# Performance work log

Hardware: AMD Instinct MI355X
Metric: run time of the kernel (lower is better)

## Reference

```python
import jax, jax.numpy as jnp
import numpy as np

TEMPERATURE = 0.07
NEG_INF = -1e9


def setup_inputs() -> dict:
    key = jax.random.key(0)
    k1, k2, k3, k4, k5 = jax.random.split(key, 5)
    B, L, H = 64, 256, 64
    query_embs = jax.random.normal(k1, (B, L, H), dtype=jnp.float32)
    key_embs = jax.random.normal(k2, (B, L, H), dtype=jnp.float32)
    labels = jax.random.randint(k3, (B,), 0, 2, dtype=jnp.int64)
    q_mask = jax.random.randint(k4, (B, L), 0, 2, dtype=jnp.int32)
    k_mask = jax.random.randint(k5, (B, L), 0, 2, dtype=jnp.int32)
    return {"query_embs": query_embs, "key_embs": key_embs, "labels": labels,
            "q_mask": q_mask, "k_mask": k_mask}


def reference(query_embs, key_embs, labels, q_mask, k_mask):
    # ColBERT-style late interaction over all B x B pairs.
    # sim: (B_q, B_k, Lq, Lk) token-level dot products.
    sim = jnp.einsum('bqh,ckh->bcqk', query_embs, key_embs)
    # Mask out padded key tokens before the max over key positions.
    sim = jnp.where(k_mask[None, :, None, :].astype(bool), sim, NEG_INF)
    maxsim = jnp.max(sim, axis=-1)                      # (B_q, B_k, Lq)
    qm = q_mask[:, None, :].astype(maxsim.dtype)        # (B_q, 1, Lq)
    scores = jnp.sum(maxsim * qm, axis=-1) / TEMPERATURE  # (B_q, B_k)
    # Cross-entropy on rows with labels==1, target = diagonal index.
    logp = jax.nn.log_softmax(scores, axis=-1)
    B = scores.shape[0]
    diag = logp[jnp.arange(B), jnp.arange(B)]           # (B,)
    w = labels.astype(scores.dtype)
    denom = jnp.maximum(jnp.sum(w), 1.0)
    return -jnp.sum(w * diag) / denom
```

## Files before the change

kernel.cpp:

```cpp
#include <hip/hip_runtime.h>
#include <math.h>

#define PB 64
#define PL 256
#define PH 64
#define TEMP 0.07f
#define NEG_INF_F (-1e9f)

#define KSTRIDE 72
#define KROWB   (KSTRIDE * 2)
#define KSLAB   (PL * KSTRIDE)
#define BGRP    4

typedef short short8 __attribute__((ext_vector_type(8)));
typedef float f32x4 __attribute__((ext_vector_type(4)));

__device__ __forceinline__ unsigned short f32_to_bf16(float f) {
    unsigned int u = __float_as_uint(f);
    u += 0x7FFFu + ((u >> 16) & 1u);
    return (unsigned short)(u >> 16);
}

__global__ __launch_bounds__(256)
void prep_kernel(const float* __restrict__ Q,
                 const float* __restrict__ K,
                 const int*   __restrict__ kmask,
                 unsigned short* __restrict__ Qb,
                 unsigned short* __restrict__ Kcomp,
                 int* __restrict__ nvK) {
    const int tid = threadIdx.x;

    if (blockIdx.x >= 256) {
        const int bb      = blockIdx.x - 256;
        const int b       = bb >> 2;
        const int quarter = bb & 3;
        const float4* src = (const float4*)(Q + (size_t)b * PL * PH) + quarter * 1024;
        unsigned short* dst = Qb + (size_t)b * PL * PH + quarter * 4096;
        #pragma unroll
        for (int it = 0; it < 4; ++it) {
            int i = it * 256 + tid;
            float4 v = src[i];
            ushort4 o;
            o.x = f32_to_bf16(v.x); o.y = f32_to_bf16(v.y);
            o.z = f32_to_bf16(v.z); o.w = f32_to_bf16(v.w);
            *(ushort4*)(dst + (size_t)i * 4) = o;
        }
        return;
    }

    const int c       = blockIdx.x >> 2;
    const int quarter = blockIdx.x & 3;
    const int lane = tid & 63;
    const int wave = tid >> 6;
    __shared__ int posArr[PL];
    __shared__ int wcnt[4];

    const int km = kmask[c * PL + tid];
    unsigned long long bal = __ballot(km != 0);
    int within = __popcll(bal & ((1ull << lane) - 1ull));
    if (lane == 0) wcnt[wave] = __popcll(bal);
    __syncthreads();
    int base = 0;
    #pragma unroll
    for (int w = 0; w < 4; ++w) base += (w < wave) ? wcnt[w] : 0;
    posArr[tid] = km ? (base + within) : -1;
    const int nv = wcnt[0] + wcnt[1] + wcnt[2] + wcnt[3];
    __syncthreads();

    unsigned short* slab = Kcomp + (size_t)c * KSLAB;
    const int sub = lane >> 4;
    const int cl  = lane & 15;

    #pragma unroll
    for (int it = 0; it < 4; ++it) {
        int r = quarter * 64 + it * 16 + wave * 4 + sub;
        int p = posArr[r];
        if (p >= 0) {
            float4 v = *(const float4*)(K + ((size_t)c * PL + r) * PH + cl * 4);
            ushort4 o;
            o.x = f32_to_bf16(v.x); o.y = f32_to_bf16(v.y);
            o.z = f32_to_bf16(v.z); o.w = f32_to_bf16(v.w);
            *(ushort4*)(slab + (size_t)p * KSTRIDE + cl * 4) = o;
        }
    }

    const int rows16 = (nv + 15) & ~15;
    const int padChunks = (rows16 - nv) * 16;
    if (tid < padChunks) {
        int row = nv + (tid >> 4);
        if (row >= quarter * 64 && row < quarter * 64 + 64) {
            *(ushort4*)(slab + (size_t)row * KSTRIDE + (tid & 15) * 4) = (ushort4){0, 0, 0, 0};
        }
    }
    if (quarter == 0 && tid == 0) nvK[c] = nv;
}

__global__ __launch_bounds__(256)
void colbert_scores_mfma(const unsigned short* __restrict__ Qb,
                         const unsigned short* __restrict__ Kcomp,
                         const int*   __restrict__ nvK,
                         const int*   __restrict__ qmask,
                         float*       __restrict__ scores) {
    const int c  = blockIdx.x;
    const int bg = blockIdx.y;
    const int tid  = threadIdx.x;
    const int wave = tid >> 6;
    const int lane = tid & 63;
    const int n    = lane & 15;
    const int g    = (lane >> 4) & 3;

    __shared__ __align__(16) unsigned short Ks[PL * KSTRIDE];
    __shared__ float red[BGRP][4];

    const int nv     = nvK[c];
    const int rows16 = (nv + 15) & ~15;
    const int nbytes = rows16 * KROWB;

    {
        const char* gsrc  = (const char*)(Kcomp + (size_t)c * KSLAB);
        char*       lbase = (char*)Ks;
        const int nchunks = (nbytes + 4095) >> 12;
        for (int it = 0; it < nchunks; ++it) {
            int off = it * 4096 + tid * 16;
            __builtin_amdgcn_global_load_lds(
                (const __attribute__((address_space(1))) unsigned int*)(gsrc + off),
                (__attribute__((address_space(3)))       unsigned int*)(lbase + off),
                16, 0, 0);
        }
    }

    __syncthreads();

    const f32x4 ZERO4 = (f32x4){0.f, 0.f, 0.f, 0.f};
    const int ntFull   = nv >> 4;
    const int tailCols = nv & 15;
    const int qw0 = wave * 64;
    const unsigned short* krow0 = &Ks[n * KSTRIDE + g * 8];

    #pragma unroll 1
    for (int bi = 0; bi < BGRP; ++bi) {
        const int b = bg * BGRP + bi;

        short8 afrag[4][2];
        {
            const unsigned short* Qrow = Qb + ((size_t)b * PL) * PH;
            #pragma unroll
            for (int rt = 0; rt < 4; ++rt) {
                const unsigned short* p = Qrow + (size_t)(qw0 + rt * 16 + n) * PH + g * 8;
                afrag[rt][0] = *(const short8*)(p);
                afrag[rt][1] = *(const short8*)(p + 32);
            }
        }

        float maxv[4][4];
        #pragma unroll
        for (int rt = 0; rt < 4; ++rt)
            #pragma unroll
            for (int r = 0; r < 4; ++r) maxv[rt][r] = NEG_INF_F;

        int ct = 0;
        for (; ct + 1 < ntFull; ct += 2) {
            const unsigned short* ka = krow0 + ct * 16 * KSTRIDE;
            short8 kA0 = *(const short8*)(ka);
            short8 kA1 = *(const short8*)(ka + 32);
            short8 kB0 = *(const short8*)(ka + 16 * KSTRIDE);
            short8 kB1 = *(const short8*)(ka + 16 * KSTRIDE + 32);

            f32x4 accA[4], accB[4];
            #pragma unroll
            for (int rt = 0; rt < 4; ++rt) {
                accA[rt] = __builtin_amdgcn_mfma_f32_16x16x32_bf16(afrag[rt][0], kA0, ZERO4, 0, 0, 0);
                accB[rt] = __builtin_amdgcn_mfma_f32_16x16x32_bf16(afrag[rt][0], kB0, ZERO4, 0, 0, 0);
            }
            #pragma unroll
            for (int rt = 0; rt < 4; ++rt) {
                accA[rt] = __builtin_amdgcn_mfma_f32_16x16x32_bf16(afrag[rt][1], kA1, accA[rt], 0, 0, 0);
                accB[rt] = __builtin_amdgcn_mfma_f32_16x16x32_bf16(afrag[rt][1], kB1, accB[rt], 0, 0, 0);
            }
            #pragma unroll
            for (int rt = 0; rt < 4; ++rt)
                #pragma unroll
                for (int r = 0; r < 4; ++r)
                    maxv[rt][r] = fmaxf(maxv[rt][r], fmaxf(accA[rt][r], accB[rt][r]));
        }

        if (ntFull & 1) {
            const unsigned short* ka = krow0 + ct * 16 * KSTRIDE;
            short8 k0 = *(const short8*)(ka);
            short8 k1 = *(const short8*)(ka + 32);
            f32x4 acc[4];
            #pragma unroll
            for (int rt = 0; rt < 4; ++rt)
                acc[rt] = __builtin_amdgcn_mfma_f32_16x16x32_bf16(afrag[rt][0], k0, ZERO4, 0, 0, 0);
            #pragma unroll
            for (int rt = 0; rt < 4; ++rt)
                acc[rt] = __builtin_amdgcn_mfma_f32_16x16x32_bf16(afrag[rt][1], k1, acc[rt], 0, 0, 0);
            #pragma unroll
            for (int rt = 0; rt < 4; ++rt)
                #pragma unroll
                for (int r = 0; r < 4; ++r)
                    maxv[rt][r] = fmaxf(maxv[rt][r], acc[rt][r]);
            ct++;
        }

        if (tailCols) {
            float biasv = (n < tailCols) ? 0.0f : NEG_INF_F;
            f32x4 BIAS4 = (f32x4){biasv, biasv, biasv, biasv};
            const unsigned short* ka = krow0 + ct * 16 * KSTRIDE;
            short8 k0 = *(const short8*)(ka);
            short8 k1 = *(const short8*)(ka + 32);
            f32x4 acc[4];
            #pragma unroll
            for (int rt = 0; rt < 4; ++rt)
                acc[rt] = __builtin_amdgcn_mfma_f32_16x16x32_bf16(afrag[rt][0], k0, BIAS4, 0, 0, 0);
            #pragma unroll
            for (int rt = 0; rt < 4; ++rt)
                acc[rt] = __builtin_amdgcn_mfma_f32_16x16x32_bf16(afrag[rt][1], k1, acc[rt], 0, 0, 0);
            #pragma unroll
            for (int rt = 0; rt < 4; ++rt)
                #pragma unroll
                for (int r = 0; r < 4; ++r)
                    maxv[rt][r] = fmaxf(maxv[rt][r], acc[rt][r]);
        }

        #pragma unroll
        for (int rt = 0; rt < 4; ++rt)
            #pragma unroll
            for (int r = 0; r < 4; ++r) {
                float mv = maxv[rt][r];
                mv = fmaxf(mv, __shfl_xor(mv, 1, 16));
                mv = fmaxf(mv, __shfl_xor(mv, 2, 16));
                mv = fmaxf(mv, __shfl_xor(mv, 4, 16));
                mv = fmaxf(mv, __shfl_xor(mv, 8, 16));
                maxv[rt][r] = mv;
            }

        float partial = 0.0f;
        if (n == 0) {
            const int* qm = qmask + b * PL;
            #pragma unroll
            for (int rt = 0; rt < 4; ++rt)
                #pragma unroll
                for (int r = 0; r < 4; ++r) {
                    int row = qw0 + rt * 16 + g * 4 + r;
                    partial += maxv[rt][r] * (float)qm[row];
                }
        }
        partial += __shfl_xor(partial, 16, 64);
        partial += __shfl_xor(partial, 32, 64);
        if (lane == 0) red[bi][wave] = partial;
    }

    __syncthreads();
    if (tid < BGRP) {
        float total = red[tid][0] + red[tid][1] + red[tid][2] + red[tid][3];
        scores[(bg * BGRP + tid) * PB + c] = total * (1.0f / TEMP);
    }
}

__global__ void finalize_kernel(const float* __restrict__ scores,
                                const int*   __restrict__ labels,
                                float*       __restrict__ out) {
    const int r = threadIdx.x;
    const float* row = scores + r * PB;
    float mx = NEG_INF_F;
    for (int j = 0; j < PB; ++j) mx = fmaxf(mx, row[j]);
    float se = 0.0f;
    for (int j = 0; j < PB; ++j) se += expf(row[j] - mx);
    float logp_diag = row[r] - mx - logf(se);
    float w = (float)labels[r];
    float wd = w * logp_diag;
    #pragma unroll
    for (int off = 32; off >= 1; off >>= 1) {
        wd += __shfl_xor(wd, off, 64);
        w  += __shfl_xor(w,  off, 64);
    }
    if (r == 0) out[0] = -wd / fmaxf(w, 1.0f);
}

extern "C" void kernel_launch(void* const* d_in, const int* in_sizes, int n_in,
                              void* d_out, int out_size, void* d_ws, size_t ws_size,
                              hipStream_t stream) {
    const float* Q      = (const float*)d_in[0];
    const float* K      = (const float*)d_in[1];
    const int*   labels = (const int*)d_in[2];
    const int*   qmask  = (const int*)d_in[3];
    const int*   kmask  = (const int*)d_in[4];
    float*       out    = (float*)d_out;

    char* ws = (char*)d_ws;
    float*          scores = (float*)ws;
    unsigned short* Qb     = (unsigned short*)(ws + 16 * 1024);
    unsigned short* Kcomp  = (unsigned short*)(ws + 16 * 1024 + 2 * 1024 * 1024);
    int*            nvK    = (int*)(ws + 16 * 1024 + 2 * 1024 * 1024 + (size_t)PB * KSLAB * 2);

    prep_kernel<<<512, 256, 0, stream>>>(Q, K, kmask, Qb, Kcomp, nvK);

    dim3 grid(PB, PB / BGRP);
    colbert_scores_mfma<<<grid, 256, 0, stream>>>(Qb, Kcomp, nvK, qmask, scores);
    finalize_kernel<<<1, 64, 0, stream>>>(scores, labels, out);
}
```

Before: 105.9 us.

## Compact masked query tokens and skip padded query tiles in MFMA scoring

The prep kernel now compacts query rows by q_mask, the same way key rows were already compacted, and zero-pads the remainder. It records per-batch valid-query counts. The scoring kernel processes only 32-row query tiles up to the larger valid count of each pair of queries, and drops the per-row mask multiply. It also halves the batch group to 2, which doubles the grid to 64x32. This skips roughly half the MFMA work on padded query tokens. The cost is a 32-row tile granularity and more blocks that each reload the K slab into LDS.

```diff
diff --git a/kernel.cpp b/kernel.cpp
--- a/kernel.cpp
+++ b/kernel.cpp
@@ -10,7 +10,7 @@
 #define KSTRIDE 72
 #define KROWB   (KSTRIDE * 2)
 #define KSLAB   (PL * KSTRIDE)
-#define BGRP    4
+#define BGRP    2
 
 typedef short short8 __attribute__((ext_vector_type(8)));
 typedef float f32x4 __attribute__((ext_vector_type(4)));
@@ -25,37 +25,24 @@
 void prep_kernel(const float* __restrict__ Q,
                  const float* __restrict__ K,
                  const int*   __restrict__ kmask,
-                 unsigned short* __restrict__ Qb,
+                 const int*   __restrict__ qmask,
+                 unsigned short* __restrict__ Qcomp,
                  unsigned short* __restrict__ Kcomp,
-                 int* __restrict__ nvK) {
-    const int tid = threadIdx.x;
-
-    if (blockIdx.x >= 256) {
-        const int bb      = blockIdx.x - 256;
-        const int b       = bb >> 2;
-        const int quarter = bb & 3;
-        const float4* src = (const float4*)(Q + (size_t)b * PL * PH) + quarter * 1024;
-        unsigned short* dst = Qb + (size_t)b * PL * PH + quarter * 4096;
-        #pragma unroll
-        for (int it = 0; it < 4; ++it) {
-            int i = it * 256 + tid;
-            float4 v = src[i];
-            ushort4 o;
-            o.x = f32_to_bf16(v.x); o.y = f32_to_bf16(v.y);
-            o.z = f32_to_bf16(v.z); o.w = f32_to_bf16(v.w);
-            *(ushort4*)(dst + (size_t)i * 4) = o;
-        }
-        return;
-    }
-
-    const int c       = blockIdx.x >> 2;
-    const int quarter = blockIdx.x & 3;
+                 int* __restrict__ nvK,
+                 int* __restrict__ nvQ) {
+    const int tid  = threadIdx.x;
     const int lane = tid & 63;
     const int wave = tid >> 6;
     __shared__ int posArr[PL];
     __shared__ int wcnt[4];
 
-    const int km = kmask[c * PL + tid];
+    const bool isQ = (blockIdx.x >= 256);
+    const int  bid = isQ ? (blockIdx.x - 256) : blockIdx.x;
+    const int  idx     = bid >> 2;
+    const int  quarter = bid & 3;
+
+    const int* mask = isQ ? (qmask + idx * PL) : (kmask + idx * PL);
+    const int km = mask[tid];
     unsigned long long bal = __ballot(km != 0);
     int within = __popcll(bal & ((1ull << lane) - 1ull));
     if (lane == 0) wcnt[wave] = __popcll(bal);
@@ -67,39 +54,62 @@
     const int nv = wcnt[0] + wcnt[1] + wcnt[2] + wcnt[3];
     __syncthreads();
 
-    unsigned short* slab = Kcomp + (size_t)c * KSLAB;
     const int sub = lane >> 4;
     const int cl  = lane & 15;
-
-    #pragma unroll
-    for (int it = 0; it < 4; ++it) {
-        int r = quarter * 64 + it * 16 + wave * 4 + sub;
-        int p = posArr[r];
-        if (p >= 0) {
-            float4 v = *(const float4*)(K + ((size_t)c * PL + r) * PH + cl * 4);
-            ushort4 o;
-            o.x = f32_to_bf16(v.x); o.y = f32_to_bf16(v.y);
-            o.z = f32_to_bf16(v.z); o.w = f32_to_bf16(v.w);
-            *(ushort4*)(slab + (size_t)p * KSTRIDE + cl * 4) = o;
-        }
-    }
-
-    const int rows16 = (nv + 15) & ~15;
-    const int padChunks = (rows16 - nv) * 16;
-    if (tid < padChunks) {
-        int row = nv + (tid >> 4);
-        if (row >= quarter * 64 && row < quarter * 64 + 64) {
-            *(ushort4*)(slab + (size_t)row * KSTRIDE + (tid & 15) * 4) = (ushort4){0, 0, 0, 0};
-        }
-    }
-    if (quarter == 0 && tid == 0) nvK[c] = nv;
+    const float* src = (isQ ? Q : K) + (size_t)idx * PL * PH;
+
+    if (!isQ) {
+        unsigned short* slab = Kcomp + (size_t)idx * KSLAB;
+        #pragma unroll
+        for (int it = 0; it < 4; ++it) {
+            int r = quarter * 64 + it * 16 + wave * 4 + sub;
+            int p = posArr[r];
+            if (p >= 0) {
+                float4 v = *(const float4*)(src + (size_t)r * PH + cl * 4);
+                ushort4 o;
+                o.x = f32_to_bf16(v.x); o.y = f32_to_bf16(v.y);
+                o.z = f32_to_bf16(v.z); o.w = f32_to_bf16(v.w);
+                *(ushort4*)(slab + (size_t)p * KSTRIDE + cl * 4) = o;
+            }
+        }
+        const int rows16 = (nv + 15) & ~15;
+        const int padChunks = (rows16 - nv) * 16;
+        if (tid < padChunks) {
+            int row = nv + (tid >> 4);
+            if (row >= quarter * 64 && row < quarter * 64 + 64)
+                *(ushort4*)(slab + (size_t)row * KSTRIDE + (tid & 15) * 4) = (ushort4){0, 0, 0, 0};
+        }
+        if (quarter == 0 && tid == 0) nvK[idx] = nv;
+    } else {
+        unsigned short* slab = Qcomp + (size_t)idx * PL * PH;
+        #pragma unroll
+        for (int it = 0; it < 4; ++it) {
+            int r = quarter * 64 + it * 16 + wave * 4 + sub;
+            int p = posArr[r];
+            if (p >= 0) {
+                float4 v = *(const float4*)(src + (size_t)r * PH + cl * 4);
+                ushort4 o;
+                o.x = f32_to_bf16(v.x); o.y = f32_to_bf16(v.y);
+                o.z = f32_to_bf16(v.z); o.w = f32_to_bf16(v.w);
+                *(ushort4*)(slab + (size_t)p * PH + cl * 4) = o;
+            }
+        }
+        #pragma unroll
+        for (int it = 0; it < 4; ++it) {
+            int id2 = it * 256 + tid;
+            int row = quarter * 64 + (id2 >> 4);
+            if (row >= nv)
+                *(ushort4*)(slab + (size_t)row * PH + (id2 & 15) * 4) = (ushort4){0, 0, 0, 0};
+        }
+        if (quarter == 0 && tid == 0) nvQ[idx] = nv;
+    }
 }
 
 __global__ __launch_bounds__(256)
-void colbert_scores_mfma(const unsigned short* __restrict__ Qb,
+void colbert_scores_mfma(const unsigned short* __restrict__ Qcomp,
                          const unsigned short* __restrict__ Kcomp,
                          const int*   __restrict__ nvK,
-                         const int*   __restrict__ qmask,
+                         const int*   __restrict__ nvQ,
                          float*       __restrict__ scores) {
     const int c  = blockIdx.x;
     const int bg = blockIdx.y;
@@ -129,34 +139,40 @@
         }
     }
 
+    const int b0 = bg * BGRP;
+    const int nq0 = nvQ[b0];
+    const int nq1 = nvQ[b0 + 1];
+    const int ntQP = ((max(nq0, nq1)) + 31) >> 5;
+
     __syncthreads();
 
     const f32x4 ZERO4 = (f32x4){0.f, 0.f, 0.f, 0.f};
     const int ntFull   = nv >> 4;
     const int tailCols = nv & 15;
-    const int qw0 = wave * 64;
     const unsigned short* krow0 = &Ks[n * KSTRIDE + g * 8];
-
-    #pragma unroll 1
-    for (int bi = 0; bi < BGRP; ++bi) {
-        const int b = bg * BGRP + bi;
-
-        short8 afrag[4][2];
-        {
-            const unsigned short* Qrow = Qb + ((size_t)b * PL) * PH;
-            #pragma unroll
-            for (int rt = 0; rt < 4; ++rt) {
-                const unsigned short* p = Qrow + (size_t)(qw0 + rt * 16 + n) * PH + g * 8;
-                afrag[rt][0] = *(const short8*)(p);
-                afrag[rt][1] = *(const short8*)(p + 32);
-            }
-        }
-
-        float maxv[4][4];
-        #pragma unroll
-        for (int rt = 0; rt < 4; ++rt)
-            #pragma unroll
-            for (int r = 0; r < 4; ++r) maxv[rt][r] = NEG_INF_F;
+    const float biasv = (n < tailCols) ? 0.0f : NEG_INF_F;
+    const f32x4 BIAS4 = (f32x4){biasv, biasv, biasv, biasv};
+
+    float partial[BGRP] = {0.0f, 0.0f};
+
+    for (int qp = wave; qp < ntQP; qp += 4) {
+        short8 aA[BGRP][2][2];
+        #pragma unroll
+        for (int bi = 0; bi < BGRP; ++bi) {
+            const unsigned short* Qrow = Qcomp + ((size_t)(b0 + bi) * PL + qp * 32 + n) * PH + g * 8;
+            aA[bi][0][0] = *(const short8*)(Qrow);
+            aA[bi][0][1] = *(const short8*)(Qrow + 32);
+            aA[bi][1][0] = *(const short8*)(Qrow + 16 * PH);
+            aA[bi][1][1] = *(const short8*)(Qrow + 16 * PH + 32);
+        }
+
+        float maxv[BGRP][2][4];
+        #pragma unroll
+        for (int bi = 0; bi < BGRP; ++bi)
+            #pragma unroll
+            for (int t = 0; t < 2; ++t)
+                #pragma unroll
+                for (int r = 0; r < 4; ++r) maxv[bi][t][r] = NEG_INF_F;
 
         int ct = 0;
         for (; ct + 1 < ntFull; ct += 2) {
@@ -166,95 +182,80 @@
             short8 kB0 = *(const short8*)(ka + 16 * KSTRIDE);
             short8 kB1 = *(const short8*)(ka + 16 * KSTRIDE + 32);
 
-            f32x4 accA[4], accB[4];
-            #pragma unroll
-            for (int rt = 0; rt < 4; ++rt) {
-                accA[rt] = __builtin_amdgcn_mfma_f32_16x16x32_bf16(afrag[rt][0], kA0, ZERO4, 0, 0, 0);
-                accB[rt] = __builtin_amdgcn_mfma_f32_16x16x32_bf16(afrag[rt][0], kB0, ZERO4, 0, 0, 0);
-            }
-            #pragma unroll
-            for (int rt = 0; rt < 4; ++rt) {
-                accA[rt] = __builtin_amdgcn_mfma_f32_16x16x32_bf16(afrag[rt][1], kA1, accA[rt], 0, 0, 0);
-                accB[rt] = __builtin_amdgcn_mfma_f32_16x16x32_bf16(afrag[rt][1], kB1, accB[rt], 0, 0, 0);
-            }
-            #pragma unroll
-            for (int rt = 0; rt < 4; ++rt)
-                #pragma unroll
-                for (int r = 0; r < 4; ++r)
-                    maxv[rt][r] = fmaxf(maxv[rt][r], fmaxf(accA[rt][r], accB[rt][r]));
+            #pragma unroll
+            for (int bi = 0; bi < BGRP; ++bi)
+                #pragma unroll
+                for (int t = 0; t < 2; ++t) {
+                    f32x4 accA = __builtin_amdgcn_mfma_f32_16x16x32_bf16(aA[bi][t][0], kA0, ZERO4, 0, 0, 0);
+                    accA = __builtin_amdgcn_mfma_f32_16x16x32_bf16(aA[bi][t][1], kA1, accA, 0, 0, 0);
+                    f32x4 accB = __builtin_amdgcn_mfma_f32_16x16x32_bf16(aA[bi][t][0], kB0, ZERO4, 0, 0, 0);
+                    accB = __builtin_amdgcn_mfma_f32_16x16x32_bf16(aA[bi][t][1], kB1, accB, 0, 0, 0);
+                    #pragma unroll
+                    for (int r = 0; r < 4; ++r)
+                        maxv[bi][t][r] = fmaxf(maxv[bi][t][r], fmaxf(accA[r], accB[r]));
+                }
         }
 
         if (ntFull & 1) {
             const unsigned short* ka = krow0 + ct * 16 * KSTRIDE;
             short8 k0 = *(const short8*)(ka);
             short8 k1 = *(const short8*)(ka + 32);
-            f32x4 acc[4];
-            #pragma unroll
-            for (int rt = 0; rt < 4; ++rt)
-                acc[rt] = __builtin_amdgcn_mfma_f32_16x16x32_bf16(afrag[rt][0], k0, ZERO4, 0, 0, 0);
-            #pragma unroll
-            for (int rt = 0; rt < 4; ++rt)
-                acc[rt] = __builtin_amdgcn_mfma_f32_16x16x32_bf16(afrag[rt][1], k1, acc[rt], 0, 0, 0);
-            #pragma unroll
-            for (int rt = 0; rt < 4; ++rt)
-                #pragma unroll
-                for (int r = 0; r < 4; ++r)
-                    maxv[rt][r] = fmaxf(maxv[rt][r], acc[rt][r]);
+            #pragma unroll
+            for (int bi = 0; bi < BGRP; ++bi)
+                #pragma unroll
+                for (int t = 0; t < 2; ++t) {
+                    f32x4 acc = __builtin_amdgcn_mfma_f32_16x16x32_bf16(aA[bi][t][0], k0, ZERO4, 0, 0, 0);
+                    acc = __builtin_amdgcn_mfma_f32_16x16x32_bf16(aA[bi][t][1], k1, acc, 0, 0, 0);
+                    #pragma unroll
+                    for (int r = 0; r < 4; ++r)
+                        maxv[bi][t][r] = fmaxf(maxv[bi][t][r], acc[r]);
+                }
             ct++;
         }
 
         if (tailCols) {
-            float biasv = (n < tailCols) ? 0.0f : NEG_INF_F;
-            f32x4 BIAS4 = (f32x4){biasv, biasv, biasv, biasv};
             const unsigned short* ka = krow0 + ct * 16 * KSTRIDE;
             short8 k0 = *(const short8*)(ka);
             short8 k1 = *(const short8*)(ka + 32);
-            f32x4 acc[4];
-            #pragma unroll
-            for (int rt = 0; rt < 4; ++rt)
-                acc[rt] = __builtin_amdgcn_mfma_f32_16x16x32_bf16(afrag[rt][0], k0, BIAS4, 0, 0, 0);
-            #pragma unroll
-            for (int rt = 0; rt < 4; ++rt)
-                acc[rt] = __builtin_amdgcn_mfma_f32_16x16x32_bf16(afrag[rt][1], k1, acc[rt], 0, 0, 0);
-            #pragma unroll
-            for (int rt = 0; rt < 4; ++rt)
-                #pragma unroll
-                for (int r = 0; r < 4; ++r)
-                    maxv[rt][r] = fmaxf(maxv[rt][r], acc[rt][r]);
-        }
-
-        #pragma unroll
-        for (int rt = 0; rt < 4; ++rt)
-            #pragma unroll
-            for (int r = 0; r < 4; ++r) {
-                float mv = maxv[rt][r];
-                mv = fmaxf(mv, __shfl_xor(mv, 1, 16));
-                mv = fmaxf(mv, __shfl_xor(mv, 2, 16));
-                mv = fmaxf(mv, __shfl_xor(mv, 4, 16));
-                mv = fmaxf(mv, __shfl_xor(mv, 8, 16));
-                maxv[rt][r] = mv;
-            }
-
-        float partial = 0.0f;
-        if (n == 0) {
-            const int* qm = qmask + b * PL;
-            #pragma unroll
-            for (int rt = 0; rt < 4; ++rt)
+            #pragma unroll
+            for (int bi = 0; bi < BGRP; ++bi)
+                #pragma unroll
+                for (int t = 0; t < 2; ++t) {
+                    f32x4 acc = __builtin_amdgcn_mfma_f32_16x16x32_bf16(aA[bi][t][0], k0, BIAS4, 0, 0, 0);
+                    acc = __builtin_amdgcn_mfma_f32_16x16x32_bf16(aA[bi][t][1], k1, acc, 0, 0, 0);
+                    #pragma unroll
+                    for (int r = 0; r < 4; ++r)
+                        maxv[bi][t][r] = fmaxf(maxv[bi][t][r], acc[r]);
+                }
+        }
+
+        #pragma unroll
+        for (int bi = 0; bi < BGRP; ++bi)
+            #pragma unroll
+            for (int t = 0; t < 2; ++t)
                 #pragma unroll
                 for (int r = 0; r < 4; ++r) {
-                    int row = qw0 + rt * 16 + g * 4 + r;
-                    partial += maxv[rt][r] * (float)qm[row];
+                    float mv = maxv[bi][t][r];
+                    mv = fmaxf(mv, __shfl_xor(mv, 1, 16));
+                    mv = fmaxf(mv, __shfl_xor(mv, 2, 16));
+                    mv = fmaxf(mv, __shfl_xor(mv, 4, 16));
+                    mv = fmaxf(mv, __shfl_xor(mv, 8, 16));
+                    if (n == 0) partial[bi] += mv;
                 }
-        }
-        partial += __shfl_xor(partial, 16, 64);
-        partial += __shfl_xor(partial, 32, 64);
-        if (lane == 0) red[bi][wave] = partial;
+    }
+
+    #pragma unroll
+    for (int bi = 0; bi < BGRP; ++bi) {
+        float p = partial[bi];
+        p += __shfl_xor(p, 16, 64);
+        p += __shfl_xor(p, 32, 64);
+        if (lane == 0) red[bi][wave] = p;
     }
 
     __syncthreads();
     if (tid < BGRP) {
         float total = red[tid][0] + red[tid][1] + red[tid][2] + red[tid][3];
-        scores[(bg * BGRP + tid) * PB + c] = total * (1.0f / TEMP);
+        scores[(b0 + tid) * PB + c] = total * (1.0f / TEMP);
     }
 }
 
@@ -290,13 +291,14 @@
 
     char* ws = (char*)d_ws;
     float*          scores = (float*)ws;
-    unsigned short* Qb     = (unsigned short*)(ws + 16 * 1024);
+    unsigned short* Qcomp  = (unsigned short*)(ws + 16 * 1024);
     unsigned short* Kcomp  = (unsigned short*)(ws + 16 * 1024 + 2 * 1024 * 1024);
     int*            nvK    = (int*)(ws + 16 * 1024 + 2 * 1024 * 1024 + (size_t)PB * KSLAB * 2);
-
-    prep_kernel<<<512, 256, 0, stream>>>(Q, K, kmask, Qb, Kcomp, nvK);
+    int*            nvQ    = nvK + 64;
+
+    prep_kernel<<<512, 256, 0, stream>>>(Q, K, kmask, qmask, Qcomp, Kcomp, nvK, nvQ);
 
     dim3 grid(PB, PB / BGRP);
-    colbert_scores_mfma<<<grid, 256, 0, stream>>>(Qb, Kcomp, nvK, qmask, scores);
+    colbert_scores_mfma<<<grid, 256, 0, stream>>>(Qcomp, Kcomp, nvK, nvQ, scores);
     finalize_kernel<<<1, 64, 0, stream>>>(scores, labels, out);
 }
```

New measurement: 96.18 us. 9.2% less time.
